# Kernel optimization log

Hardware: AMD Instinct MI355X
Metric: run time of the kernel (lower is better)

## Reference

```python
import jax, jax.numpy as jnp
import numpy as np
from math import log2

B, F, C, H, W = 4, 16, 3, 96, 128
P = 8
HP, WP = H // P, W // P            # 12, 16
N = HP * WP                        # 192 spatial tokens
DIM, HEADS, DH = 512, 8, 64
INNER = HEADS * DH                 # 512
DEPTH = 4
FFH = DIM * 4                      # 2048 (GEGLU output half)
SCALE = DH ** -0.5


def _rotate_every_two(x):
    # pairs adjacent elements: (x0,x1) -> (-x1, x0)
    x1 = x[..., ::2]
    x2 = x[..., 1::2]
    return jnp.stack((-x2, x1), axis=-1).reshape(x.shape)


def _rope(t, sin, cos):
    return t * cos + _rotate_every_two(t) * sin


def _frame_rot():
    # RotaryEmbedding(DH): freqs concatenated (not interleaved)
    inv = 1.0 / (10000.0 ** (jnp.arange(0, DH, 2, dtype=jnp.float32) / DH))  # (32,)
    freqs = jnp.arange(F, dtype=jnp.float32)[:, None] * inv[None, :]          # (F,32)
    freqs = jnp.concatenate([freqs, freqs], axis=-1)                          # (F,64)
    return jnp.sin(freqs), jnp.cos(freqs)


def _image_rot():
    # AxialRotaryEmbedding(DH), max_freq=10; interleaved repeat (d j), j=2
    d4 = DH // 4
    scales = 2.0 ** jnp.linspace(0.0, log2(10.0 / 2.0), d4)                   # (16,)
    hs = jnp.linspace(-1.0, 1.0, HP)[:, None] * scales * jnp.pi              # (HP,16)
    ws = jnp.linspace(-1.0, 1.0, WP)[:, None] * scales * jnp.pi              # (WP,16)
    xs = jnp.broadcast_to(hs[:, None, :], (HP, WP, d4))
    ys = jnp.broadcast_to(ws[None, :, :], (HP, WP, d4))
    sin = jnp.concatenate([jnp.sin(xs), jnp.sin(ys)], axis=-1).reshape(N, DH // 2)
    cos = jnp.concatenate([jnp.cos(xs), jnp.cos(ys)], axis=-1).reshape(N, DH // 2)
    return jnp.repeat(sin, 2, axis=-1), jnp.repeat(cos, 2, axis=-1)           # (N,64)


def _ln(x, g, b):
    mu = x.mean(-1, keepdims=True)
    var = ((x - mu) ** 2).mean(-1, keepdims=True)
    return (x - mu) * jax.lax.rsqrt(var + 1e-5) * g + b


def _split_heads(t):
    # (B, F*N, HEADS*DH) -> (B, HEADS, F, N, DH); head dim is outer in (h d)
    return t.reshape(B, F, N, HEADS, DH).transpose(0, 3, 1, 2, 4)


def _merge_heads(t):
    # (B, HEADS, F, N, DH) -> (B, F*N, HEADS*DH)
    return t.transpose(0, 2, 3, 1, 4).reshape(B, F * N, INNER)


def _attention(y, wqkv, wo, bo, sin, cos, over_time):
    q, k, v = jnp.split(y @ wqkv, 3, axis=-1)
    q = q * SCALE
    q, k, v = map(_split_heads, (q, k, v))  # (B,h,F,N,DH)
    if over_time:
        s, c = sin[:, None, :], cos[:, None, :]     # broadcast over N
        q, k = _rope(q, s, c), _rope(k, s, c)
        sim = jnp.einsum('bhind,bhjnd->bhnij', q, k)
        a = jax.nn.softmax(sim, axis=-1)
        o = jnp.einsum('bhnij,bhjnd->bhind', a, v)
    else:
        q, k = _rope(q, sin, cos), _rope(k, sin, cos)  # sin/cos (N,DH)
        sim = jnp.einsum('bhfid,bhfjd->bhfij', q, k)
        a = jax.nn.softmax(sim, axis=-1)
        o = jnp.einsum('bhfij,bhfjd->bhfid', a, v)
    return _merge_heads(o) @ wo + bo


def _forward(video, patch_w, patch_b, ln_t_g, ln_t_b, ln_s_g, ln_s_b,
             ln_f_g, ln_f_b, qkv_t, out_t_w, out_t_b, qkv_s, out_s_w,
             out_s_b, ff_w1, ff_b1, ff_w2, ff_b2):
    # patchify: b f c (hp p1) (wp p2) -> b (f hp wp) (p1 p2 c)
    v = video.reshape(B, F, C, HP, P, WP, P).transpose(0, 1, 3, 5, 4, 6, 2)
    v = v.reshape(B, F * N, P * P * C)
    x = v @ patch_w + patch_b                       # (B, F*N, DIM)

    fsin, fcos = _frame_rot()
    isin, icos = _image_rot()

    for l in range(DEPTH):
        y = _ln(x, ln_t_g[l], ln_t_b[l])
        x = x + _attention(y, qkv_t[l], out_t_w[l], out_t_b[l], fsin, fcos, True)
        y = _ln(x, ln_s_g[l], ln_s_b[l])
        x = x + _attention(y, qkv_s[l], out_s_w[l], out_s_b[l], isin, icos, False)
        y = _ln(x, ln_f_g[l], ln_f_b[l])
        h1 = y @ ff_w1[l] + ff_b1[l]
        a, g = jnp.split(h1, 2, axis=-1)
        x = x + (a * jax.nn.gelu(g, approximate=False)) @ ff_w2[l] + ff_b2[l]
    return x


def setup_inputs() -> dict:
    key = jax.random.key(0)
    ks = jax.random.split(key, 10)
    s = 0.02
    return {
        'video': jax.random.normal(ks[0], (B, F, C, H, W), jnp.float32),
        'patch_w': jax.random.normal(ks[1], (C * P * P, DIM), jnp.float32) * s,
        'patch_b': jnp.zeros((DIM,), jnp.float32),
        'ln_t_g': jnp.ones((DEPTH, DIM), jnp.float32),
        'ln_t_b': jnp.zeros((DEPTH, DIM), jnp.float32),
        'ln_s_g': jnp.ones((DEPTH, DIM), jnp.float32),
        'ln_s_b': jnp.zeros((DEPTH, DIM), jnp.float32),
        'ln_f_g': jnp.ones((DEPTH, DIM), jnp.float32),
        'ln_f_b': jnp.zeros((DEPTH, DIM), jnp.float32),
        'qkv_t': jax.random.normal(ks[2], (DEPTH, DIM, 3 * INNER), jnp.float32) * s,
        'out_t_w': jax.random.normal(ks[3], (DEPTH, INNER, DIM), jnp.float32) * s,
        'out_t_b': jnp.zeros((DEPTH, DIM), jnp.float32),
        'qkv_s': jax.random.normal(ks[4], (DEPTH, DIM, 3 * INNER), jnp.float32) * s,
        'out_s_w': jax.random.normal(ks[5], (DEPTH, INNER, DIM), jnp.float32) * s,
        'out_s_b': jnp.zeros((DEPTH, DIM), jnp.float32),
        'ff_w1': jax.random.normal(ks[6], (DEPTH, DIM, 2 * FFH), jnp.float32) * s,
        'ff_b1': jnp.zeros((DEPTH, 2 * FFH), jnp.float32),
        'ff_w2': jax.random.normal(ks[7], (DEPTH, FFH, DIM), jnp.float32) * s,
        'ff_b2': jnp.zeros((DEPTH, DIM), jnp.float32),
    }


def reference(video, patch_w, patch_b, ln_t_g, ln_t_b, ln_s_g, ln_s_b,
              ln_f_g, ln_f_b, qkv_t, out_t_w, out_t_b, qkv_s, out_s_w,
              out_s_b, ff_w1, ff_b1, ff_w2, ff_b2):
    return _forward(video, patch_w, patch_b, ln_t_g, ln_t_b, ln_s_g, ln_s_b,
                    ln_f_g, ln_f_b, qkv_t, out_t_w, out_t_b, qkv_s, out_s_w,
                    out_s_b, ff_w1, ff_b1, ff_w2, ff_b2)
```

## Files before the change

kernel.cpp:

```cpp
#include <hip/hip_runtime.h>
#include <math.h>

#define B_ 4
#define F_ 16
#define HP_ 12
#define WP_ 16
#define N_ 192
#define S_ (F_*N_)
#define ROWS (B_*S_)
#define DIM_ 512
#define HEADS_ 8
#define DH_ 64
#define FFH_ 2048
#define PATCH_K 192
#define PI_F 3.14159265358979323846f

typedef unsigned short u16;
typedef __attribute__((ext_vector_type(8))) short bf16x8;
typedef __attribute__((ext_vector_type(4))) float f32x4;

__device__ __forceinline__ u16 bf16_rne(float f) {
    unsigned int u = __float_as_uint(f);
    u += 0x7FFFu + ((u >> 16) & 1u);
    return (u16)(u >> 16);
}
__device__ __forceinline__ float bf16_f32(u16 h) {
    return __uint_as_float(((unsigned int)h) << 16);
}

__device__ __forceinline__ void swz2d(int& bx, int& by) {
    int gx = gridDim.x;
    int nwg = gx * gridDim.y;
    int id = by * gx + bx;
    if ((nwg & 7) == 0) {
        int cpx = nwg >> 3;
        int wg = (id & 7) * cpx + (id >> 3);
        bx = wg % gx;
        by = wg / gx;
    }
}

__global__ void rope_tables(float* __restrict__ fsin, float* __restrict__ fcos,
                            float* __restrict__ isin, float* __restrict__ icos) {
    int tid = blockIdx.x * blockDim.x + threadIdx.x;
    int stride = gridDim.x * blockDim.x;
    for (int idx = tid; idx < F_ * 64; idx += stride) {
        int f = idx >> 6, j = idx & 63;
        int i = j & 31;
        float inv = powf(10000.0f, -((float)i) / 32.0f);
        float fr = (float)f * inv;
        fsin[idx] = sinf(fr);
        fcos[idx] = cosf(fr);
    }
    for (int idx = tid; idx < N_ * 32; idx += stride) {
        int n = idx >> 5, k = idx & 31;
        int h = n / WP_, w = n % WP_;
        float scale = exp2f((float)(k & 15) * (log2f(5.0f) / 15.0f));
        float pos = (k < 16) ? (-1.0f + 2.0f * (float)h / (float)(HP_ - 1))
                             : (-1.0f + 2.0f * (float)w / (float)(WP_ - 1));
        float val = pos * scale * PI_F;
        float sv = sinf(val), cv = cosf(val);
        isin[n * 64 + 2 * k] = sv; isin[n * 64 + 2 * k + 1] = sv;
        icos[n * 64 + 2 * k] = cv; icos[n * 64 + 2 * k + 1] = cv;
    }
}

__global__ void rearrange_video_p(const float* __restrict__ video,
                                  u16* __restrict__ Vh, u16* __restrict__ Vl) {
    int t = blockIdx.x * blockDim.x + threadIdx.x;
    const int total = ROWS * PATCH_K;
    if (t >= total) return;
    int col = t % PATCH_K;
    int row = t / PATCH_K;
    int c  = col % 3;
    int pp = col / 3;
    int pi = pp >> 3, pj = pp & 7;
    int n  = row % N_;
    int bf = row / N_;
    int hp = n / WP_, wp = n % WP_;
    int hidx = hp * 8 + pi, widx = wp * 8 + pj;
    float f = video[((size_t)(bf * 3 + c) * 96 + hidx) * 128 + widx];
    u16 h = bf16_rne(f);
    Vh[t] = h;
    Vl[t] = bf16_rne(f - bf16_f32(h));
}

__global__ __launch_bounds__(256) void convert_wt(
    const float* __restrict__ W, u16* __restrict__ Wh, u16* __restrict__ Wl,
    int K, int N) {
    __shared__ float tile[32][33];
    int nb = blockIdx.x * 32, kb = blockIdx.y * 32;
    int tx = threadIdx.x & 31, ty = threadIdx.x >> 5;
    #pragma unroll
    for (int i = 0; i < 32; i += 8)
        tile[ty + i][tx] = W[(size_t)(kb + ty + i) * N + nb + tx];
    __syncthreads();
    #pragma unroll
    for (int i = 0; i < 32; i += 8) {
        int n = nb + ty + i, k = kb + tx;
        float f = tile[tx][ty + i];
        u16 h = bf16_rne(f);
        Wh[(size_t)n * K + k] = h;
        Wl[(size_t)n * K + k] = bf16_rne(f - bf16_f32(h));
    }
}

__global__ __launch_bounds__(64) void layernorm_p(
    const float* __restrict__ x, const float* __restrict__ g,
    const float* __restrict__ b, u16* __restrict__ Yh, u16* __restrict__ Yl) {
    int row = blockIdx.x;
    int lane = threadIdx.x;
    const float* xr = x + (size_t)row * DIM_;
    float4 v0 = *(const float4*)&xr[lane * 8];
    float4 v1 = *(const float4*)&xr[lane * 8 + 4];
    float s  = v0.x + v0.y + v0.z + v0.w + v1.x + v1.y + v1.z + v1.w;
    float sq = v0.x*v0.x + v0.y*v0.y + v0.z*v0.z + v0.w*v0.w
             + v1.x*v1.x + v1.y*v1.y + v1.z*v1.z + v1.w*v1.w;
    for (int off = 32; off; off >>= 1) { s += __shfl_xor(s, off); sq += __shfl_xor(sq, off); }
    float mu  = s * (1.0f / 512.0f);
    float var = sq * (1.0f / 512.0f) - mu * mu;
    float inv = rsqrtf(var + 1e-5f);
    float4 g0 = *(const float4*)&g[lane * 8];
    float4 g1 = *(const float4*)&g[lane * 8 + 4];
    float4 b0 = *(const float4*)&b[lane * 8];
    float4 b1 = *(const float4*)&b[lane * 8 + 4];
    float o[8];
    o[0] = (v0.x - mu) * inv * g0.x + b0.x;
    o[1] = (v0.y - mu) * inv * g0.y + b0.y;
    o[2] = (v0.z - mu) * inv * g0.z + b0.z;
    o[3] = (v0.w - mu) * inv * g0.w + b0.w;
    o[4] = (v1.x - mu) * inv * g1.x + b1.x;
    o[5] = (v1.y - mu) * inv * g1.y + b1.y;
    o[6] = (v1.z - mu) * inv * g1.z + b1.z;
    o[7] = (v1.w - mu) * inv * g1.w + b1.w;
    size_t ro = (size_t)row * DIM_ + lane * 8;
    ushort4 h0, h1, l0, l1;
    h0.x = bf16_rne(o[0]); l0.x = bf16_rne(o[0] - bf16_f32(h0.x));
    h0.y = bf16_rne(o[1]); l0.y = bf16_rne(o[1] - bf16_f32(h0.y));
    h0.z = bf16_rne(o[2]); l0.z = bf16_rne(o[2] - bf16_f32(h0.z));
    h0.w = bf16_rne(o[3]); l0.w = bf16_rne(o[3] - bf16_f32(h0.w));
    h1.x = bf16_rne(o[4]); l1.x = bf16_rne(o[4] - bf16_f32(h1.x));
    h1.y = bf16_rne(o[5]); l1.y = bf16_rne(o[5] - bf16_f32(h1.y));
    h1.z = bf16_rne(o[6]); l1.z = bf16_rne(o[6] - bf16_f32(h1.z));
    h1.w = bf16_rne(o[7]); l1.w = bf16_rne(o[7] - bf16_f32(h1.w));
    *(ushort4*)&Yh[ro]     = h0;
    *(ushort4*)&Yh[ro + 4] = h1;
    *(ushort4*)&Yl[ro]     = l0;
    *(ushort4*)&Yl[ro + 4] = l1;
}

template<int EPI>
__global__ __launch_bounds__(256) void gemm_mfma3(
    const u16* __restrict__ Ah, const u16* __restrict__ Al,
    const u16* __restrict__ Wh, const u16* __restrict__ Wl,
    const float* __restrict__ bias, float* __restrict__ C,
    int M, int N, int K) {
    __shared__ u16 As[2][128 * 40];
    __shared__ u16 Ws[2][128 * 40];
    int bx = blockIdx.x, by = blockIdx.y;
    swz2d(bx, by);
    const int bm0 = by * 128, bn0 = bx * 128;
    const int tid = threadIdx.x, lane = tid & 63, wid = tid >> 6;
    const int wm = (wid >> 1) * 64, wn = (wid & 1) * 64;
    const int fr = lane & 15, kg = (lane >> 4) * 8;
    f32x4 acc[4][4] = {};
    for (int k0 = 0; k0 < K; k0 += 32) {
        #pragma unroll
        for (int it = 0; it < 2; ++it) {
            int cc = it * 256 + tid;
            int row = cc >> 2, kc = (cc & 3) * 8;
            size_t ga = (size_t)(bm0 + row) * K + k0 + kc;
            size_t gw = (size_t)(bn0 + row) * K + k0 + kc;
            *(uint4*)&As[0][row * 40 + kc] = *(const uint4*)&Ah[ga];
            *(uint4*)&As[1][row * 40 + kc] = *(const uint4*)&Al[ga];
            *(uint4*)&Ws[0][row * 40 + kc] = *(const uint4*)&Wh[gw];
            *(uint4*)&Ws[1][row * 40 + kc] = *(const uint4*)&Wl[gw];
        }
        __syncthreads();
        bf16x8 ah[4], al[4], bh[4], bl[4];
        #pragma unroll
        for (int i = 0; i < 4; ++i) {
            ah[i] = *(const bf16x8*)&As[0][(wm + i * 16 + fr) * 40 + kg];
            al[i] = *(const bf16x8*)&As[1][(wm + i * 16 + fr) * 40 + kg];
            bh[i] = *(const bf16x8*)&Ws[0][(wn + i * 16 + fr) * 40 + kg];
            bl[i] = *(const bf16x8*)&Ws[1][(wn + i * 16 + fr) * 40 + kg];
        }
        #pragma unroll
        for (int i = 0; i < 4; ++i)
            #pragma unroll
            for (int j = 0; j < 4; ++j) {
                acc[i][j] = __builtin_amdgcn_mfma_f32_16x16x32_bf16(ah[i], bh[j], acc[i][j], 0, 0, 0);
                acc[i][j] = __builtin_amdgcn_mfma_f32_16x16x32_bf16(ah[i], bl[j], acc[i][j], 0, 0, 0);
                acc[i][j] = __builtin_amdgcn_mfma_f32_16x16x32_bf16(al[i], bh[j], acc[i][j], 0, 0, 0);
            }
        __syncthreads();
    }
    const int r0 = (lane >> 4) * 4;
    #pragma unroll
    for (int i = 0; i < 4; ++i)
        #pragma unroll
        for (int j = 0; j < 4; ++j) {
            int col = bn0 + wn + j * 16 + fr;
            float bb = bias ? bias[col] : 0.0f;
            #pragma unroll
            for (int r = 0; r < 4; ++r) {
                int row = bm0 + wm + i * 16 + r0 + r;
                float v = acc[i][j][r] + bb;
                size_t off = (size_t)row * N + col;
                if (EPI == 1) v += C[off];
                C[off] = v;
            }
        }
}

template<int EPI, int SPLITA>
__global__ __launch_bounds__(256) void gemm_n64(
    const u16* __restrict__ Ah, const u16* __restrict__ Al,
    const u16* __restrict__ Wh, const u16* __restrict__ Wl,
    const float* __restrict__ bias, float* __restrict__ C,
    int M, int N, int K) {
    __shared__ u16 As[SPLITA ? 2 : 1][128 * 40];
    __shared__ u16 Ws[2][64 * 40];
    int bx = blockIdx.x, by = blockIdx.y;
    swz2d(bx, by);
    const int bm0 = by * 128, bn0 = bx * 64;
    const int tid = threadIdx.x, lane = tid & 63, wid = tid >> 6;
    const int wm = (wid >> 1) * 64, wn = (wid & 1) * 32;
    const int fr = lane & 15, kg = (lane >> 4) * 8;
    f32x4 acc[4][2] = {};
    for (int k0 = 0; k0 < K; k0 += 32) {
        #pragma unroll
        for (int it = 0; it < 2; ++it) {
            int cc = it * 256 + tid;
            int row = cc >> 2, kc = (cc & 3) * 8;
            size_t ga = (size_t)(bm0 + row) * K + k0 + kc;
            *(uint4*)&As[0][row * 40 + kc] = *(const uint4*)&Ah[ga];
            if (SPLITA)
                *(uint4*)&As[1][row * 40 + kc] = *(const uint4*)&Al[ga];
        }
        {
            int row = tid >> 2, kc = (tid & 3) * 8;
            size_t gw = (size_t)(bn0 + row) * K + k0 + kc;
            *(uint4*)&Ws[0][row * 40 + kc] = *(const uint4*)&Wh[gw];
            *(uint4*)&Ws[1][row * 40 + kc] = *(const uint4*)&Wl[gw];
        }
        __syncthreads();
        bf16x8 ah[4], al[4], bh[2], bl[2];
        #pragma unroll
        for (int i = 0; i < 4; ++i) {
            ah[i] = *(const bf16x8*)&As[0][(wm + i * 16 + fr) * 40 + kg];
            if (SPLITA)
                al[i] = *(const bf16x8*)&As[1][(wm + i * 16 + fr) * 40 + kg];
        }
        #pragma unroll
        for (int j = 0; j < 2; ++j) {
            bh[j] = *(const bf16x8*)&Ws[0][(wn + j * 16 + fr) * 40 + kg];
            bl[j] = *(const bf16x8*)&Ws[1][(wn + j * 16 + fr) * 40 + kg];
        }
        #pragma unroll
        for (int i = 0; i < 4; ++i)
            #pragma unroll
            for (int j = 0; j < 2; ++j) {
                acc[i][j] = __builtin_amdgcn_mfma_f32_16x16x32_bf16(ah[i], bh[j], acc[i][j], 0, 0, 0);
                acc[i][j] = __builtin_amdgcn_mfma_f32_16x16x32_bf16(ah[i], bl[j], acc[i][j], 0, 0, 0);
                if (SPLITA)
                    acc[i][j] = __builtin_amdgcn_mfma_f32_16x16x32_bf16(al[i], bh[j], acc[i][j], 0, 0, 0);
            }
        __syncthreads();
    }
    const int r0 = (lane >> 4) * 4;
    #pragma unroll
    for (int i = 0; i < 4; ++i)
        #pragma unroll
        for (int j = 0; j < 2; ++j) {
            int col = bn0 + wn + j * 16 + fr;
            float bb = bias ? bias[col] : 0.0f;
            #pragma unroll
            for (int r = 0; r < 4; ++r) {
                int row = bm0 + wm + i * 16 + r0 + r;
                float v = acc[i][j][r] + bb;
                size_t off = (size_t)row * N + col;
                if (EPI == 1) v += C[off];
                C[off] = v;
            }
        }
}

__global__ __launch_bounds__(256) void gemm_glu3(
    const u16* __restrict__ Ah, const u16* __restrict__ Al,
    const u16* __restrict__ Wh, const u16* __restrict__ Wl,
    const float* __restrict__ bias, u16* __restrict__ Hh) {
    const int K = DIM_;
    __shared__ u16 As[2][128 * 40];
    __shared__ u16 Ws[2][128 * 40];
    int bx = blockIdx.x, by = blockIdx.y;
    swz2d(bx, by);
    const int bm0 = by * 128, bn0 = bx * 64;
    const int tid = threadIdx.x, lane = tid & 63, wid = tid >> 6;
    const int wm = (wid >> 1) * 64, wn2 = (wid & 1) * 32;
    const int fr = lane & 15, kg = (lane >> 4) * 8;
    f32x4 acca[4][2] = {}, accg[4][2] = {};
    for (int k0 = 0; k0 < K; k0 += 32) {
        #pragma unroll
        for (int it = 0; it < 2; ++it) {
            int cc = it * 256 + tid;
            int row = cc >> 2, kc = (cc & 3) * 8;
            size_t ga = (size_t)(bm0 + row) * K + k0 + kc;
            int ng = (row < 64) ? (bn0 + row) : (FFH_ + bn0 + row - 64);
            size_t gw = (size_t)ng * K + k0 + kc;
            *(uint4*)&As[0][row * 40 + kc] = *(const uint4*)&Ah[ga];
            *(uint4*)&As[1][row * 40 + kc] = *(const uint4*)&Al[ga];
            *(uint4*)&Ws[0][row * 40 + kc] = *(const uint4*)&Wh[gw];
            *(uint4*)&Ws[1][row * 40 + kc] = *(const uint4*)&Wl[gw];
        }
        __syncthreads();
        bf16x8 ah[4], al[4], bah[2], bal[2], bgh[2], bgl[2];
        #pragma unroll
        for (int i = 0; i < 4; ++i) {
            ah[i] = *(const bf16x8*)&As[0][(wm + i * 16 + fr) * 40 + kg];
            al[i] = *(const bf16x8*)&As[1][(wm + i * 16 + fr) * 40 + kg];
        }
        #pragma unroll
        for (int j = 0; j < 2; ++j) {
            bah[j] = *(const bf16x8*)&Ws[0][(wn2 + j * 16 + fr) * 40 + kg];
            bal[j] = *(const bf16x8*)&Ws[1][(wn2 + j * 16 + fr) * 40 + kg];
            bgh[j] = *(const bf16x8*)&Ws[0][(64 + wn2 + j * 16 + fr) * 40 + kg];
            bgl[j] = *(const bf16x8*)&Ws[1][(64 + wn2 + j * 16 + fr) * 40 + kg];
        }
        #pragma unroll
        for (int i = 0; i < 4; ++i)
            #pragma unroll
            for (int j = 0; j < 2; ++j) {
                acca[i][j] = __builtin_amdgcn_mfma_f32_16x16x32_bf16(ah[i], bah[j], acca[i][j], 0, 0, 0);
                acca[i][j] = __builtin_amdgcn_mfma_f32_16x16x32_bf16(ah[i], bal[j], acca[i][j], 0, 0, 0);
                acca[i][j] = __builtin_amdgcn_mfma_f32_16x16x32_bf16(al[i], bah[j], acca[i][j], 0, 0, 0);
                accg[i][j] = __builtin_amdgcn_mfma_f32_16x16x32_bf16(ah[i], bgh[j], accg[i][j], 0, 0, 0);
                accg[i][j] = __builtin_amdgcn_mfma_f32_16x16x32_bf16(ah[i], bgl[j], accg[i][j], 0, 0, 0);
                accg[i][j] = __builtin_amdgcn_mfma_f32_16x16x32_bf16(al[i], bgh[j], accg[i][j], 0, 0, 0);
            }
        __syncthreads();
    }
    const int r0 = (lane >> 4) * 4;
    #pragma unroll
    for (int i = 0; i < 4; ++i)
        #pragma unroll
        for (int j = 0; j < 2; ++j) {
            int col = bn0 + wn2 + j * 16 + fr;
            float ba = bias[col], bg = bias[FFH_ + col];
            #pragma unroll
            for (int r = 0; r < 4; ++r) {
                int row = bm0 + wm + i * 16 + r0 + r;
                float av = acca[i][j][r] + ba;
                float gv = accg[i][j][r] + bg;
                float gl = 0.5f * gv * (1.0f + erff(gv * 0.70710678118654752f));
                Hh[(size_t)row * FFH_ + col] = bf16_rne(av * gl);
            }
        }
}

__global__ __launch_bounds__(64) void attn_time(
    const float* __restrict__ qkv, const float* __restrict__ fsin,
    const float* __restrict__ fcos, u16* __restrict__ Oh, u16* __restrict__ Ol) {
    int bid = blockIdx.x;
    int n = bid % N_;
    int h = (bid / N_) % HEADS_;
    int b = bid / (N_ * HEADS_);
    int lane = threadIdx.x;
    __shared__ float qs[16][68], ks[16][68], vs[16][68], Pm[16][16];
    int parity = lane & 1;
    for (int f = 0; f < F_; ++f) {
        size_t base = (size_t)(b * S_ + f * N_ + n) * 1536 + h * 64;
        float qv = qkv[base + lane] * 0.125f;
        float kv = qkv[base + 512 + lane];
        float vv = qkv[base + 1024 + lane];
        float sn = fsin[f * 64 + lane], cs = fcos[f * 64 + lane];
        float qx = __shfl_xor(qv, 1);
        float kx = __shfl_xor(kv, 1);
        float qrot = parity ? qx : -qx;
        float krot = parity ? kx : -kx;
        qs[f][lane] = qv * cs + qrot * sn;
        ks[f][lane] = kv * cs + krot * sn;
        vs[f][lane] = vv;
    }
    __syncthreads();
    int j = lane & 15, r = lane >> 4;
    for (int rr = 0; rr < 4; ++rr) {
        int i = rr * 4 + r;
        float sacc = 0.f;
        #pragma unroll
        for (int d4 = 0; d4 < 16; ++d4) {
            float4 qa = *(const float4*)&qs[i][d4 * 4];
            float4 ka = *(const float4*)&ks[j][d4 * 4];
            sacc += qa.x*ka.x + qa.y*ka.y + qa.z*ka.z + qa.w*ka.w;
        }
        float mx = sacc;
        for (int off = 8; off; off >>= 1) mx = fmaxf(mx, __shfl_xor(mx, off));
        float p = expf(sacc - mx);
        float sum = p;
        for (int off = 8; off; off >>= 1) sum += __shfl_xor(sum, off);
        Pm[i][j] = p / sum;
    }
    __syncthreads();
    for (int i = 0; i < 16; ++i) {
        float acc = 0.f;
        #pragma unroll
        for (int jj = 0; jj < 16; ++jj) acc += Pm[i][jj] * vs[jj][lane];
        size_t ob = (size_t)(b * S_ + i * N_ + n) * 512 + h * 64 + lane;
        u16 hh = bf16_rne(acc);
        Oh[ob] = hh;
        Ol[ob] = bf16_rne(acc - bf16_f32(hh));
    }
}

__global__ __launch_bounds__(256, 2) void attn_space_mfma(
    const float* __restrict__ qkv, const float* __restrict__ isin,
    const float* __restrict__ icos, u16* __restrict__ Oh, u16* __restrict__ Ol) {
    int bid = blockIdx.x;
    int f = bid % F_;
    int h = (bid / F_) % HEADS_;
    int b = bid / (F_ * HEADS_);
    const int tid = threadIdx.x, lane = tid & 63, wid = tid >> 6;
    const int fr = lane & 15, g = lane >> 4;
    __shared__ u16 Ksh[32][72], Ksl[32][72];
    __shared__ u16 Vsh[64][40], Vsl[64][40];
    __shared__ u16 Psh[4][48][40], Psl[4][48][40];
    const size_t rowbase = (size_t)b * S_ + (size_t)f * N_;

    bf16x8 qh[3][2], ql[3][2];
    #pragma unroll
    for (int i = 0; i < 3; ++i) {
        int n = wid * 48 + i * 16 + fr;
        #pragma unroll
        for (int ks = 0; ks < 2; ++ks) {
            int dbase = ks * 32 + g * 8;
            const float* qp = &qkv[(rowbase + n) * 1536 + h * 64 + dbase];
            float4 t0 = *(const float4*)qp;
            float4 t1 = *(const float4*)(qp + 4);
            float4 s0 = *(const float4*)&isin[n * 64 + dbase];
            float4 s1 = *(const float4*)&isin[n * 64 + dbase + 4];
            float4 c0 = *(const float4*)&icos[n * 64 + dbase];
            float4 c1 = *(const float4*)&icos[n * 64 + dbase + 4];
            float v[8];
            v[0] = (t0.x * c0.x - t0.y * s0.x) * 0.125f;
            v[1] = (t0.y * c0.y + t0.x * s0.y) * 0.125f;
            v[2] = (t0.z * c0.z - t0.w * s0.z) * 0.125f;
            v[3] = (t0.w * c0.w + t0.z * s0.w) * 0.125f;
            v[4] = (t1.x * c1.x - t1.y * s1.x) * 0.125f;
            v[5] = (t1.y * c1.y + t1.x * s1.y) * 0.125f;
            v[6] = (t1.z * c1.z - t1.w * s1.z) * 0.125f;
            v[7] = (t1.w * c1.w + t1.z * s1.w) * 0.125f;
            bf16x8 hh, ll;
            #pragma unroll
            for (int e = 0; e < 8; ++e) {
                u16 hb = bf16_rne(v[e]);
                hh[e] = (short)hb;
                ll[e] = (short)bf16_rne(v[e] - bf16_f32(hb));
            }
            qh[i][ks] = hh; ql[i][ks] = ll;
        }
    }

    float m[3][4], l[3][4];
    f32x4 oacc[3][4] = {};
    #pragma unroll
    for (int i = 0; i < 3; ++i)
        #pragma unroll
        for (int r = 0; r < 4; ++r) { m[i][r] = -3.0e38f; l[i][r] = 0.0f; }

    for (int kt = 0; kt < 6; ++kt) {
        __syncthreads();
        #pragma unroll
        for (int it = 0; it < 2; ++it) {
            int c = it * 256 + tid;
            int kr = c >> 4, dseg = (c & 15) * 4;
            int nk = kt * 32 + kr;
            float4 t = *(const float4*)&qkv[(rowbase + nk) * 1536 + 512 + h * 64 + dseg];
            float4 sn = *(const float4*)&isin[nk * 64 + dseg];
            float4 cs = *(const float4*)&icos[nk * 64 + dseg];
            float v0 = t.x * cs.x - t.y * sn.x;
            float v1 = t.y * cs.y + t.x * sn.y;
            float v2 = t.z * cs.z - t.w * sn.z;
            float v3 = t.w * cs.w + t.z * sn.w;
            ushort4 hh, ll;
            hh.x = bf16_rne(v0); ll.x = bf16_rne(v0 - bf16_f32(hh.x));
            hh.y = bf16_rne(v1); ll.y = bf16_rne(v1 - bf16_f32(hh.y));
            hh.z = bf16_rne(v2); ll.z = bf16_rne(v2 - bf16_f32(hh.z));
            hh.w = bf16_rne(v3); ll.w = bf16_rne(v3 - bf16_f32(hh.w));
            *(ushort4*)&Ksh[kr][dseg] = hh;
            *(ushort4*)&Ksl[kr][dseg] = ll;
        }
        {
            int kr = tid & 31, ds8 = tid >> 5;
            const float* vp = &qkv[(rowbase + kt * 32 + kr) * 1536 + 1024 + h * 64 + ds8 * 8];
            float4 a = *(const float4*)vp;
            float4 b4 = *(const float4*)(vp + 4);
            float vv[8] = {a.x, a.y, a.z, a.w, b4.x, b4.y, b4.z, b4.w};
            #pragma unroll
            for (int e = 0; e < 8; ++e) {
                u16 hb = bf16_rne(vv[e]);
                Vsh[ds8 * 8 + e][kr] = hb;
                Vsl[ds8 * 8 + e][kr] = bf16_rne(vv[e] - bf16_f32(hb));
            }
        }
        __syncthreads();
        bf16x8 kbh[2][2], kbl[2][2];
        #pragma unroll
        for (int j = 0; j < 2; ++j)
            #pragma unroll
            for (int ks = 0; ks < 2; ++ks) {
                kbh[j][ks] = *(const bf16x8*)&Ksh[j * 16 + fr][ks * 32 + g * 8];
                kbl[j][ks] = *(const bf16x8*)&Ksl[j * 16 + fr][ks * 32 + g * 8];
            }
        f32x4 s[3][2] = {};
        #pragma unroll
        for (int i = 0; i < 3; ++i)
            #pragma unroll
            for (int j = 0; j < 2; ++j)
                #pragma unroll
                for (int ks = 0; ks < 2; ++ks) {
                    s[i][j] = __builtin_amdgcn_mfma_f32_16x16x32_bf16(qh[i][ks], kbh[j][ks], s[i][j], 0, 0, 0);
                    s[i][j] = __builtin_amdgcn_mfma_f32_16x16x32_bf16(qh[i][ks], kbl[j][ks], s[i][j], 0, 0, 0);
                    s[i][j] = __builtin_amdgcn_mfma_f32_16x16x32_bf16(ql[i][ks], kbh[j][ks], s[i][j], 0, 0, 0);
                }
        #pragma unroll
        for (int i = 0; i < 3; ++i) {
            float tmax[4], mn[4], corr[4], psum[4];
            #pragma unroll
            for (int r = 0; r < 4; ++r) tmax[r] = fmaxf(s[i][0][r], s[i][1][r]);
            #pragma unroll
            for (int off = 8; off; off >>= 1)
                #pragma unroll
                for (int r = 0; r < 4; ++r) tmax[r] = fmaxf(tmax[r], __shfl_xor(tmax[r], off));
            float p0[4], p1[4];
            #pragma unroll
            for (int r = 0; r < 4; ++r) {
                mn[r] = fmaxf(m[i][r], tmax[r]);
                corr[r] = expf(m[i][r] - mn[r]);
                p0[r] = expf(s[i][0][r] - mn[r]);
                p1[r] = expf(s[i][1][r] - mn[r]);
                psum[r] = p0[r] + p1[r];
                m[i][r] = mn[r];
            }
            #pragma unroll
            for (int off = 8; off; off >>= 1)
                #pragma unroll
                for (int r = 0; r < 4; ++r) psum[r] += __shfl_xor(psum[r], off);
            #pragma unroll
            for (int r = 0; r < 4; ++r) l[i][r] = l[i][r] * corr[r] + psum[r];
            #pragma unroll
            for (int dj = 0; dj < 4; ++dj)
                #pragma unroll
                for (int r = 0; r < 4; ++r) oacc[i][dj][r] *= corr[r];
            #pragma unroll
            for (int r = 0; r < 4; ++r) {
                int rl = i * 16 + g * 4 + r;
                u16 h0 = bf16_rne(p0[r]);
                Psh[wid][rl][fr]      = h0;
                Psl[wid][rl][fr]      = bf16_rne(p0[r] - bf16_f32(h0));
                u16 h1 = bf16_rne(p1[r]);
                Psh[wid][rl][16 + fr] = h1;
                Psl[wid][rl][16 + fr] = bf16_rne(p1[r] - bf16_f32(h1));
            }
        }
        bf16x8 pah[3], pal[3];
        #pragma unroll
        for (int i = 0; i < 3; ++i) {
            pah[i] = *(const bf16x8*)&Psh[wid][i * 16 + fr][g * 8];
            pal[i] = *(const bf16x8*)&Psl[wid][i * 16 + fr][g * 8];
        }
        bf16x8 vbh[4], vbl[4];
        #pragma unroll
        for (int dj = 0; dj < 4; ++dj) {
            vbh[dj] = *(const bf16x8*)&Vsh[dj * 16 + fr][g * 8];
            vbl[dj] = *(const bf16x8*)&Vsl[dj * 16 + fr][g * 8];
        }
        #pragma unroll
        for (int i = 0; i < 3; ++i)
            #pragma unroll
            for (int dj = 0; dj < 4; ++dj) {
                oacc[i][dj] = __builtin_amdgcn_mfma_f32_16x16x32_bf16(pah[i], vbh[dj], oacc[i][dj], 0, 0, 0);
                oacc[i][dj] = __builtin_amdgcn_mfma_f32_16x16x32_bf16(pah[i], vbl[dj], oacc[i][dj], 0, 0, 0);
                oacc[i][dj] = __builtin_amdgcn_mfma_f32_16x16x32_bf16(pal[i], vbh[dj], oacc[i][dj], 0, 0, 0);
            }
    }
    #pragma unroll
    for (int i = 0; i < 3; ++i) {
        #pragma unroll
        for (int r = 0; r < 4; ++r) {
            int row = wid * 48 + i * 16 + g * 4 + r;
            float invl = 1.0f / l[i][r];
            #pragma unroll
            for (int dj = 0; dj < 4; ++dj) {
                float v = oacc[i][dj][r] * invl;
                size_t ob = (rowbase + row) * 512 + h * 64 + dj * 16 + fr;
                u16 hh = bf16_rne(v);
                Oh[ob] = hh;
                Ol[ob] = bf16_rne(v - bf16_f32(hh));
            }
        }
    }
}

extern "C" void kernel_launch(void* const* d_in, const int* in_sizes, int n_in,
                              void* d_out, int out_size, void* d_ws, size_t ws_size,
                              hipStream_t stream) {
    (void)in_sizes; (void)n_in; (void)out_size; (void)ws_size;
    const float* video   = (const float*)d_in[0];
    const float* patch_w = (const float*)d_in[1];
    const float* patch_b = (const float*)d_in[2];
    const float* ln_t_g  = (const float*)d_in[3];
    const float* ln_t_b  = (const float*)d_in[4];
    const float* ln_s_g  = (const float*)d_in[5];
    const float* ln_s_b  = (const float*)d_in[6];
    const float* ln_f_g  = (const float*)d_in[7];
    const float* ln_f_b  = (const float*)d_in[8];
    const float* qkv_t   = (const float*)d_in[9];
    const float* out_t_w = (const float*)d_in[10];
    const float* out_t_b = (const float*)d_in[11];
    const float* qkv_s   = (const float*)d_in[12];
    const float* out_s_w = (const float*)d_in[13];
    const float* out_s_b = (const float*)d_in[14];
    const float* ff_w1   = (const float*)d_in[15];
    const float* ff_b1   = (const float*)d_in[16];
    const float* ff_w2   = (const float*)d_in[17];
    const float* ff_b2   = (const float*)d_in[18];

    float* x = (float*)d_out;

    u16* wqt_h = (u16*)d_ws;
    u16* wqt_l = wqt_h + 1536 * 512;
    u16* wot_h = wqt_l + 1536 * 512;
    u16* wot_l = wot_h + 512 * 512;
    u16* wqs_h = wot_l + 512 * 512;
    u16* wqs_l = wqs_h + 1536 * 512;
    u16* wos_h = wqs_l + 1536 * 512;
    u16* wos_l = wos_h + 512 * 512;
    u16* wpt_h = wos_l + 512 * 512;
    u16* wpt_l = wpt_h + 512 * PATCH_K;
    u16* y_h   = wpt_l + 512 * PATCH_K;
    u16* y_l   = y_h + (size_t)ROWS * DIM_;
    float* big2 = (float*)(y_l + (size_t)ROWS * DIM_);
    float* qkv  = big2;
    u16* vp_h = (u16*)big2;
    u16* vp_l = vp_h + (size_t)ROWS * PATCH_K;
    u16* h2    = (u16*)big2;
    u16* f1t_h = h2 + (size_t)ROWS * FFH_;
    u16* f1t_l = f1t_h + 4096 * 512;
    u16* f2t_h = f1t_l + 4096 * 512;
    u16* f2t_l = f2t_h + 512 * FFH_;
    float* fsin = (float*)((char*)big2 + (size_t)ROWS * 1536 * 4);
    float* fcos = fsin + F_ * 64;
    float* isin = fcos + F_ * 64;
    float* icos = isin + N_ * 64;
    u16* o_h = y_h;
    u16* o_l = y_l;

    rope_tables<<<2, 256, 0, stream>>>(fsin, fcos, isin, icos);

    convert_wt<<<dim3(DIM_ / 32, PATCH_K / 32), 256, 0, stream>>>(patch_w, wpt_h, wpt_l, PATCH_K, DIM_);
    rearrange_video_p<<<(ROWS * PATCH_K + 255) / 256, 256, 0, stream>>>(video, vp_h, vp_l);
    gemm_n64<0, 1><<<dim3(DIM_ / 64, ROWS / 128), 256, 0, stream>>>(
        vp_h, vp_l, wpt_h, wpt_l, patch_b, x, ROWS, DIM_, PATCH_K);

    for (int l = 0; l < 4; ++l) {
        convert_wt<<<dim3(1536 / 32, DIM_ / 32), 256, 0, stream>>>(
            qkv_t + (size_t)l * DIM_ * 1536, wqt_h, wqt_l, DIM_, 1536);
        convert_wt<<<dim3(DIM_ / 32, DIM_ / 32), 256, 0, stream>>>(
            out_t_w + (size_t)l * DIM_ * DIM_, wot_h, wot_l, DIM_, DIM_);
        convert_wt<<<dim3(1536 / 32, DIM_ / 32), 256, 0, stream>>>(
            qkv_s + (size_t)l * DIM_ * 1536, wqs_h, wqs_l, DIM_, 1536);
        convert_wt<<<dim3(DIM_ / 32, DIM_ / 32), 256, 0, stream>>>(
            out_s_w + (size_t)l * DIM_ * DIM_, wos_h, wos_l, DIM_, DIM_);

        layernorm_p<<<ROWS, 64, 0, stream>>>(x, ln_t_g + l * DIM_, ln_t_b + l * DIM_, y_h, y_l);
        gemm_mfma3<0><<<dim3(1536 / 128, ROWS / 128), 256, 0, stream>>>(
            y_h, y_l, wqt_h, wqt_l, nullptr, qkv, ROWS, 1536, DIM_);
        attn_time<<<B_ * HEADS_ * N_, 64, 0, stream>>>(qkv, fsin, fcos, o_h, o_l);
        gemm_n64<1, 1><<<dim3(DIM_ / 64, ROWS / 128), 256, 0, stream>>>(
            o_h, o_l, wot_h, wot_l, out_t_b + l * DIM_, x, ROWS, DIM_, DIM_);

        layernorm_p<<<ROWS, 64, 0, stream>>>(x, ln_s_g + l * DIM_, ln_s_b + l * DIM_, y_h, y_l);
        gemm_mfma3<0><<<dim3(1536 / 128, ROWS / 128), 256, 0, stream>>>(
            y_h, y_l, wqs_h, wqs_l, nullptr, qkv, ROWS, 1536, DIM_);
        attn_space_mfma<<<B_ * HEADS_ * F_, 256, 0, stream>>>(qkv, isin, icos, o_h, o_l);
        gemm_n64<1, 1><<<dim3(DIM_ / 64, ROWS / 128), 256, 0, stream>>>(
            o_h, o_l, wos_h, wos_l, out_s_b + l * DIM_, x, ROWS, DIM_, DIM_);

        convert_wt<<<dim3(4096 / 32, DIM_ / 32), 256, 0, stream>>>(
            ff_w1 + (size_t)l * DIM_ * 2 * FFH_, f1t_h, f1t_l, DIM_, 4096);
        convert_wt<<<dim3(DIM_ / 32, FFH_ / 32), 256, 0, stream>>>(
            ff_w2 + (size_t)l * FFH_ * DIM_, f2t_h, f2t_l, FFH_, DIM_);
        layernorm_p<<<ROWS, 64, 0, stream>>>(x, ln_f_g + l * DIM_, ln_f_b + l * DIM_, y_h, y_l);
        gemm_glu3<<<dim3(FFH_ / 64, ROWS / 128), 256, 0, stream>>>(
            y_h, y_l, f1t_h, f1t_l, ff_b1 + l * 2 * FFH_, h2);
        gemm_n64<1, 0><<<dim3(DIM_ / 64, ROWS / 128), 256, 0, stream>>>(
            h2, nullptr, f2t_h, f2t_l, ff_b2 + l * DIM_, x, ROWS, DIM_, FFH_);
    }
}
```

Measured before the change: 2.542 ms.

## Drop activation low-part in GEGLU GEMM and use column-major workgroup swizzle

The FF1 GEGLU GEMM now takes only the bf16 high part of the layernormed activation, which removes one of the three split-precision MFMA products per accumulator and the low-part activation loads. The layernorm skips computing and writing the low part when given a null pointer. Separately, the workgroup swizzle for every GEMM now maps tiles column-major, so consecutive groups share weight tiles. The trade-off is reduced activation precision in the FF input, which could loosen accuracy against the fp32 reference.

```diff
diff --git a/kernel.cpp b/kernel.cpp
--- a/kernel.cpp
+++ b/kernel.cpp
@@ -28,15 +28,15 @@
     return __uint_as_float(((unsigned int)h) << 16);
 }
 
-__device__ __forceinline__ void swz2d(int& bx, int& by) {
-    int gx = gridDim.x;
-    int nwg = gx * gridDim.y;
+__device__ __forceinline__ void swz_col(int& bx, int& by) {
+    int gx = gridDim.x, gy = gridDim.y;
+    int nwg = gx * gy;
     int id = by * gx + bx;
     if ((nwg & 7) == 0) {
         int cpx = nwg >> 3;
-        int wg = (id & 7) * cpx + (id >> 3);
-        bx = wg % gx;
-        by = wg / gx;
+        int t = (id & 7) * cpx + (id >> 3);
+        bx = t / gy;
+        by = t % gy;
     }
 }
 
@@ -134,19 +134,26 @@
     o[6] = (v1.z - mu) * inv * g1.z + b1.z;
     o[7] = (v1.w - mu) * inv * g1.w + b1.w;
     size_t ro = (size_t)row * DIM_ + lane * 8;
-    ushort4 h0, h1, l0, l1;
-    h0.x = bf16_rne(o[0]); l0.x = bf16_rne(o[0] - bf16_f32(h0.x));
-    h0.y = bf16_rne(o[1]); l0.y = bf16_rne(o[1] - bf16_f32(h0.y));
-    h0.z = bf16_rne(o[2]); l0.z = bf16_rne(o[2] - bf16_f32(h0.z));
-    h0.w = bf16_rne(o[3]); l0.w = bf16_rne(o[3] - bf16_f32(h0.w));
-    h1.x = bf16_rne(o[4]); l1.x = bf16_rne(o[4] - bf16_f32(h1.x));
-    h1.y = bf16_rne(o[5]); l1.y = bf16_rne(o[5] - bf16_f32(h1.y));
-    h1.z = bf16_rne(o[6]); l1.z = bf16_rne(o[6] - bf16_f32(h1.z));
-    h1.w = bf16_rne(o[7]); l1.w = bf16_rne(o[7] - bf16_f32(h1.w));
+    ushort4 h0, h1;
+    h0.x = bf16_rne(o[0]); h0.y = bf16_rne(o[1]);
+    h0.z = bf16_rne(o[2]); h0.w = bf16_rne(o[3]);
+    h1.x = bf16_rne(o[4]); h1.y = bf16_rne(o[5]);
+    h1.z = bf16_rne(o[6]); h1.w = bf16_rne(o[7]);
     *(ushort4*)&Yh[ro]     = h0;
     *(ushort4*)&Yh[ro + 4] = h1;
-    *(ushort4*)&Yl[ro]     = l0;
-    *(ushort4*)&Yl[ro + 4] = l1;
+    if (Yl) {
+        ushort4 l0, l1;
+        l0.x = bf16_rne(o[0] - bf16_f32(h0.x));
+        l0.y = bf16_rne(o[1] - bf16_f32(h0.y));
+        l0.z = bf16_rne(o[2] - bf16_f32(h0.z));
+        l0.w = bf16_rne(o[3] - bf16_f32(h0.w));
+        l1.x = bf16_rne(o[4] - bf16_f32(h1.x));
+        l1.y = bf16_rne(o[5] - bf16_f32(h1.y));
+        l1.z = bf16_rne(o[6] - bf16_f32(h1.z));
+        l1.w = bf16_rne(o[7] - bf16_f32(h1.w));
+        *(ushort4*)&Yl[ro]     = l0;
+        *(ushort4*)&Yl[ro + 4] = l1;
+    }
 }
 
 template<int EPI>
@@ -158,7 +165,7 @@
     __shared__ u16 As[2][128 * 40];
     __shared__ u16 Ws[2][128 * 40];
     int bx = blockIdx.x, by = blockIdx.y;
-    swz2d(bx, by);
+    swz_col(bx, by);
     const int bm0 = by * 128, bn0 = bx * 128;
     const int tid = threadIdx.x, lane = tid & 63, wid = tid >> 6;
     const int wm = (wid >> 1) * 64, wn = (wid & 1) * 64;
@@ -222,7 +229,7 @@
     __shared__ u16 As[SPLITA ? 2 : 1][128 * 40];
     __shared__ u16 Ws[2][64 * 40];
     int bx = blockIdx.x, by = blockIdx.y;
-    swz2d(bx, by);
+    swz_col(bx, by);
     const int bm0 = by * 128, bn0 = bx * 64;
     const int tid = threadIdx.x, lane = tid & 63, wid = tid >> 6;
     const int wm = (wid >> 1) * 64, wn = (wid & 1) * 32;
@@ -287,14 +294,14 @@
 }
 
 __global__ __launch_bounds__(256) void gemm_glu3(
-    const u16* __restrict__ Ah, const u16* __restrict__ Al,
+    const u16* __restrict__ Ah,
     const u16* __restrict__ Wh, const u16* __restrict__ Wl,
     const float* __restrict__ bias, u16* __restrict__ Hh) {
     const int K = DIM_;
-    __shared__ u16 As[2][128 * 40];
+    __shared__ u16 As[128 * 40];
     __shared__ u16 Ws[2][128 * 40];
     int bx = blockIdx.x, by = blockIdx.y;
-    swz2d(bx, by);
+    swz_col(bx, by);
     const int bm0 = by * 128, bn0 = bx * 64;
     const int tid = threadIdx.x, lane = tid & 63, wid = tid >> 6;
     const int wm = (wid >> 1) * 64, wn2 = (wid & 1) * 32;
@@ -308,18 +315,15 @@
             size_t ga = (size_t)(bm0 + row) * K + k0 + kc;
             int ng = (row < 64) ? (bn0 + row) : (FFH_ + bn0 + row - 64);
             size_t gw = (size_t)ng * K + k0 + kc;
-            *(uint4*)&As[0][row * 40 + kc] = *(const uint4*)&Ah[ga];
-            *(uint4*)&As[1][row * 40 + kc] = *(const uint4*)&Al[ga];
+            *(uint4*)&As[row * 40 + kc] = *(const uint4*)&Ah[ga];
             *(uint4*)&Ws[0][row * 40 + kc] = *(const uint4*)&Wh[gw];
             *(uint4*)&Ws[1][row * 40 + kc] = *(const uint4*)&Wl[gw];
         }
         __syncthreads();
-        bf16x8 ah[4], al[4], bah[2], bal[2], bgh[2], bgl[2];
-        #pragma unroll
-        for (int i = 0; i < 4; ++i) {
-            ah[i] = *(const bf16x8*)&As[0][(wm + i * 16 + fr) * 40 + kg];
-            al[i] = *(const bf16x8*)&As[1][(wm + i * 16 + fr) * 40 + kg];
-        }
+        bf16x8 ah[4], bah[2], bal[2], bgh[2], bgl[2];
+        #pragma unroll
+        for (int i = 0; i < 4; ++i)
+            ah[i] = *(const bf16x8*)&As[(wm + i * 16 + fr) * 40 + kg];
         #pragma unroll
         for (int j = 0; j < 2; ++j) {
             bah[j] = *(const bf16x8*)&Ws[0][(wn2 + j * 16 + fr) * 40 + kg];
@@ -333,10 +337,8 @@
             for (int j = 0; j < 2; ++j) {
                 acca[i][j] = __builtin_amdgcn_mfma_f32_16x16x32_bf16(ah[i], bah[j], acca[i][j], 0, 0, 0);
                 acca[i][j] = __builtin_amdgcn_mfma_f32_16x16x32_bf16(ah[i], bal[j], acca[i][j], 0, 0, 0);
-                acca[i][j] = __builtin_amdgcn_mfma_f32_16x16x32_bf16(al[i], bah[j], acca[i][j], 0, 0, 0);
                 accg[i][j] = __builtin_amdgcn_mfma_f32_16x16x32_bf16(ah[i], bgh[j], accg[i][j], 0, 0, 0);
                 accg[i][j] = __builtin_amdgcn_mfma_f32_16x16x32_bf16(ah[i], bgl[j], accg[i][j], 0, 0, 0);
-                accg[i][j] = __builtin_amdgcn_mfma_f32_16x16x32_bf16(al[i], bgh[j], accg[i][j], 0, 0, 0);
             }
         __syncthreads();
     }
@@ -690,9 +692,9 @@
             ff_w1 + (size_t)l * DIM_ * 2 * FFH_, f1t_h, f1t_l, DIM_, 4096);
         convert_wt<<<dim3(DIM_ / 32, FFH_ / 32), 256, 0, stream>>>(
             ff_w2 + (size_t)l * FFH_ * DIM_, f2t_h, f2t_l, FFH_, DIM_);
-        layernorm_p<<<ROWS, 64, 0, stream>>>(x, ln_f_g + l * DIM_, ln_f_b + l * DIM_, y_h, y_l);
+        layernorm_p<<<ROWS, 64, 0, stream>>>(x, ln_f_g + l * DIM_, ln_f_b + l * DIM_, y_h, nullptr);
         gemm_glu3<<<dim3(FFH_ / 64, ROWS / 128), 256, 0, stream>>>(
-            y_h, y_l, f1t_h, f1t_l, ff_b1 + l * 2 * FFH_, h2);
+            y_h, f1t_h, f1t_l, ff_b1 + l * 2 * FFH_, h2);
         gemm_n64<1, 0><<<dim3(DIM_ / 64, ROWS / 128), 256, 0, stream>>>(
             h2, nullptr, f2t_h, f2t_l, ff_b2 + l * DIM_, x, ROWS, DIM_, FFH_);
     }
```

New measurement: 2.534 ms. No clear change (-0.3%).
